# Kernel optimization log

Measured on AMD Instinct MI355X. Metric: run time of the kernel, lower is better.

## Reference

```python
import jax, jax.numpy as jnp
import numpy as np
import math

N, L, D = 1024, 32, 768
N_OUT, IN_DIM, OUT_DIM = 16, 64, 64
EPS = 1e-8


def setup_inputs() -> dict:
    key = jax.random.key(0)
    ks = jax.random.split(key, 4)
    x = jax.random.normal(ks[0], (N, L, D), jnp.float32)
    mask = jnp.ones((N, L), jnp.float32)
    scaled = lambda k, shape, fan: jax.random.normal(k, shape, jnp.float32) * (1.0 / np.sqrt(fan).astype(np.float32))
    Wscore = scaled(ks[1], (L, D, 1), D)
    Bscore = jnp.zeros((L, 1, 1), jnp.float32)
    Wcap = scaled(ks[2], (L, D, IN_DIM), D)
    Bcap = jnp.zeros((L, 1, IN_DIM), jnp.float32)
    Wvote = scaled(ks[3], (L, N_OUT, IN_DIM, OUT_DIM), IN_DIM)
    Bvote = jnp.zeros((L, N_OUT, 1, OUT_DIM), jnp.float32)
    beta_use = jnp.zeros((L, 1, 1, 1), jnp.float32)
    beta_ign = jnp.zeros((1, N_OUT, 1, 1), jnp.float32)
    return dict(x=x, mask=mask, Wscore=Wscore, Bscore=Bscore, Wcap=Wcap,
                Bcap=Bcap, Wvote=Wvote, Bvote=Bvote, beta_use=beta_use,
                beta_ign=beta_ign, iters=3)


def reference(x, mask, Wscore, Bscore, Wcap, Bcap, Wvote, Bvote, beta_use, beta_ign, iters):
    n_out = Wvote.shape[1]
    half_pi = np.float32(0.5 * math.pi)
    x_t = jnp.transpose(x, (1, 0, 2))                      # [L, N, D]
    a_in = jnp.matmul(x_t, Wscore) + Bscore                # [L, N, 1]
    mu_in = jax.nn.gelu(jnp.matmul(x_t, Wcap) + Bcap, approximate=False)  # [L, N, in_dim]
    f_a_in = jax.nn.sigmoid(a_in) * jnp.transpose(mask)[..., None]        # [L, N, 1]
    f_a_in = f_a_in[:, None, :, :]                         # [L, 1, N, 1]
    # votes: [L, n_out, N, out_dim] (einsum avoids materializing repeated mu_in)
    V = jnp.einsum('lni,lkio->lkno', mu_in, Wvote) + Bvote

    R = jnp.full((1, n_out, 1, 1), 1.0 / n_out, dtype=x.dtype)
    a_out = mu_out = var_out = None
    for t in range(iters):
        if t > 0:
            log_p = (-jnp.sum((V - mu_out[None]) ** 2 / (2.0 * var_out[None] + EPS), axis=-1)
                     - 1.0 - half_pi
                     - 0.5 * jnp.sum(jnp.log(var_out[None] + EPS), axis=-1))   # [L, n_out, N]
            R = jax.nn.softmax(jax.nn.log_sigmoid(a_out)[None] + log_p[..., None], axis=1)
        D_use = f_a_in * R                                  # [L, n_out, N, 1]
        D_ign = f_a_in - D_use
        a_out = jnp.sum(beta_use * D_use, axis=0) - jnp.sum(beta_ign * D_ign, axis=0)  # [n_out, N, 1]
        denom = jnp.sum(D_use, axis=0) + EPS                # [n_out, N, 1]
        mu_out = jnp.sum(D_use * V, axis=0) / denom         # [n_out, N, out_dim]
        var_out = jnp.sum(D_use * (V - mu_out[None]) ** 2, axis=0) / denom

    a_fin = jnp.transpose(a_out[..., 0])                    # [N, n_out]
    mu_fin = jnp.transpose(mu_out, (1, 0, 2))               # [N, n_out, out_dim]
    return a_fin, mu_fin
```

## Files before the change

### kernel.cpp

```cpp
#include <hip/hip_runtime.h>
#include <hip/hip_bf16.h>

#define L_DIM 32
#define N_DIM 1024
#define D_DIM 768
#define K_DIM 16
#define I_DIM 64
#define O_DIM 64
#define EPSF 1e-8f
#define PX 72

typedef unsigned short u16;
typedef __attribute__((ext_vector_type(8))) short short8;
typedef __attribute__((ext_vector_type(4))) float f32x4;
#define MFMA __builtin_amdgcn_mfma_f32_16x16x32_bf16

__device__ __forceinline__ float bf2f(u16 v) {
    union { unsigned int u; float f; } x; x.u = ((unsigned int)v) << 16; return x.f;
}
__device__ __forceinline__ u16 f2bf(float f) {
    union { float f; unsigned int u; } x; x.f = f;
    unsigned int u = x.u;
    u += 0x7FFFu + ((u >> 16) & 1u);
    return (u16)(u >> 16);
}
__device__ __forceinline__ void split2(float v, u16& h, u16& l) {
    u16 hh = f2bf(v);
    h = hh;
    l = f2bf(v - bf2f(hh));
}

__global__ __launch_bounds__(256) void prep_wcap(
    const float* __restrict__ W, u16* __restrict__ H, u16* __restrict__ Lo)
{
    const int l = blockIdx.y, d0 = blockIdx.x * 64, t = threadIdx.x;
    __shared__ float tile[64][65];
    #pragma unroll
    for (int p = 0; p < 4; p++) {
        int dd = p * 16 + (t >> 4), i4 = (t & 15) * 4;
        float4 v = *(const float4*)&W[((size_t)l * D_DIM + d0 + dd) * I_DIM + i4];
        tile[dd][i4] = v.x; tile[dd][i4+1] = v.y; tile[dd][i4+2] = v.z; tile[dd][i4+3] = v.w;
    }
    __syncthreads();
    #pragma unroll
    for (int p = 0; p < 4; p++) {
        int i = p * 16 + (t >> 4), dd0 = (t & 15) * 4;
        u16 h[4], lo[4];
        #pragma unroll
        for (int j = 0; j < 4; j++) split2(tile[dd0 + j][i], h[j], lo[j]);
        size_t base = ((size_t)l * I_DIM + i) * D_DIM + d0 + dd0;
        uint2 ph; ph.x = h[0] | ((unsigned)h[1] << 16); ph.y = h[2] | ((unsigned)h[3] << 16);
        uint2 pl; pl.x = lo[0] | ((unsigned)lo[1] << 16); pl.y = lo[2] | ((unsigned)lo[3] << 16);
        *(uint2*)&H[base] = ph;
        *(uint2*)&Lo[base] = pl;
    }
}

__global__ __launch_bounds__(256) void prep_wvote(
    const float* __restrict__ W, u16* __restrict__ H, u16* __restrict__ Lo)
{
    const int l = blockIdx.y, k = blockIdx.x, t = threadIdx.x;
    __shared__ float tile[64][65];
    #pragma unroll
    for (int p = 0; p < 4; p++) {
        int i = p * 16 + (t >> 4), o4 = (t & 15) * 4;
        float4 v = *(const float4*)&W[(((size_t)l * K_DIM + k) * I_DIM + i) * O_DIM + o4];
        tile[i][o4] = v.x; tile[i][o4+1] = v.y; tile[i][o4+2] = v.z; tile[i][o4+3] = v.w;
    }
    __syncthreads();
    #pragma unroll
    for (int p = 0; p < 4; p++) {
        int o = p * 16 + (t >> 4), i0 = (t & 15) * 4;
        u16 h[4], lo[4];
        #pragma unroll
        for (int j = 0; j < 4; j++) split2(tile[i0 + j][o], h[j], lo[j]);
        size_t base = (((size_t)l * K_DIM + k) * O_DIM + o) * I_DIM + i0;
        uint2 ph; ph.x = h[0] | ((unsigned)h[1] << 16); ph.y = h[2] | ((unsigned)h[3] << 16);
        uint2 pl; pl.x = lo[0] | ((unsigned)lo[1] << 16); pl.y = lo[2] | ((unsigned)lo[3] << 16);
        *(uint2*)&H[base] = ph;
        *(uint2*)&Lo[base] = pl;
    }
}

__global__ __launch_bounds__(256) void kernelA(
    const float* __restrict__ x, const float* __restrict__ mask,
    const float* __restrict__ Wscore, const float* __restrict__ Bscore,
    const u16* __restrict__ WcH, const u16* __restrict__ WcL,
    const float* __restrict__ Bcap,
    float* __restrict__ mu_out, float* __restrict__ fa_out,
    int nbase, int nchunk)
{
    const int l   = blockIdx.y;
    const int n0l = blockIdx.x * 32;
    const int t    = threadIdx.x;
    const int w    = t >> 6;
    const int lane = t & 63;
    const int quad = lane >> 4;
    const int ln16 = lane & 15;

    __shared__ u16 xh[32][PX], xl[32][PX];
    __shared__ float wsc_s[64];
    __shared__ float bcap_s[64];

    if (t < 64) bcap_s[t] = Bcap[l * I_DIM + t];

    f32x4 acc[2] = {{0.f,0.f,0.f,0.f},{0.f,0.f,0.f,0.f}};
    float apart = 0.f;

    for (int ch = 0; ch < 12; ch++) {
        const int k0 = ch * 64;
        __syncthreads();
        #pragma unroll
        for (int p = 0; p < 2; p++) {
            int n = p * 16 + (t >> 4), d0 = (t & 15) * 4;
            float4 v = *(const float4*)&x[((size_t)(nbase + n0l + n) * L_DIM + l) * D_DIM + k0 + d0];
            u16 h[4], lo[4];
            split2(v.x, h[0], lo[0]); split2(v.y, h[1], lo[1]);
            split2(v.z, h[2], lo[2]); split2(v.w, h[3], lo[3]);
            uint2 ph; ph.x = h[0] | ((unsigned)h[1] << 16); ph.y = h[2] | ((unsigned)h[3] << 16);
            uint2 pl; pl.x = lo[0] | ((unsigned)lo[1] << 16); pl.y = lo[2] | ((unsigned)lo[3] << 16);
            *(uint2*)&xh[n][d0] = ph;
            *(uint2*)&xl[n][d0] = pl;
        }
        if (t < 64) wsc_s[t] = Wscore[l * D_DIM + k0 + t];
        __syncthreads();

        {
            const int n = t >> 3, s8 = (t & 7) * 8;
            float ss = 0.f;
            #pragma unroll
            for (int j = 0; j < 8; j++) {
                int dd = s8 + j;
                ss += (bf2f(xh[n][dd]) + bf2f(xl[n][dd])) * wsc_s[dd];
            }
            apart += ss;
        }

        #pragma unroll
        for (int ks = 0; ks < 2; ks++) {
            const int kk = ks * 32;
            size_t wbase = ((size_t)l * I_DIM + (w * 16 + ln16)) * D_DIM + k0 + kk + quad * 8;
            short8 ah = *(const short8*)&WcH[wbase];
            short8 al = *(const short8*)&WcL[wbase];
            #pragma unroll
            for (int c = 0; c < 2; c++) {
                const int n = c * 16 + ln16;
                short8 bh = *(const short8*)&xh[n][kk + quad * 8];
                short8 bl = *(const short8*)&xl[n][kk + quad * 8];
                acc[c] = MFMA(ah, bh, acc[c], 0, 0, 0);
                acc[c] = MFMA(ah, bl, acc[c], 0, 0, 0);
                acc[c] = MFMA(al, bh, acc[c], 0, 0, 0);
            }
        }
    }

    apart += __shfl_xor(apart, 1, 64);
    apart += __shfl_xor(apart, 2, 64);
    apart += __shfl_xor(apart, 4, 64);
    if ((t & 7) == 0) {
        int n = t >> 3;
        float a = apart + Bscore[l];
        float sig = 1.f / (1.f + expf(-a));
        float m = mask[(size_t)(nbase + n0l + n) * L_DIM + l];
        fa_out[(size_t)l * nchunk + n0l + n] = sig * m;
    }

    #pragma unroll
    for (int c = 0; c < 2; c++) {
        const int n = c * 16 + ln16;
        const int i0 = w * 16 + quad * 4;
        float4 o;
        float* op = (float*)&o;
        #pragma unroll
        for (int r = 0; r < 4; r++) {
            float v = acc[c][r] + bcap_s[i0 + r];
            op[r] = 0.5f * v * (1.f + erff(v * 0.70710678118f));
        }
        *(float4*)&mu_out[((size_t)l * nchunk + n0l + n) * I_DIM + i0] = o;
    }
}

__global__ __launch_bounds__(256) void kernelB(
    const float* __restrict__ mu_in,
    const u16* __restrict__ WvH, const u16* __restrict__ WvL,
    const float* __restrict__ Bvote,
    float* __restrict__ V, int nchunk)
{
    const int l   = blockIdx.z;
    const int k   = blockIdx.y;
    const int n0l = blockIdx.x * 64;
    const int t    = threadIdx.x;
    const int w    = t >> 6;
    const int lane = t & 63;
    const int quad = lane >> 4;
    const int ln16 = lane & 15;

    __shared__ u16 mh[64][PX], ml[64][PX];
    __shared__ float bvote_s[64];

    if (t < 64) bvote_s[t] = Bvote[((size_t)l * K_DIM + k) * O_DIM + t];

    #pragma unroll
    for (int p = 0; p < 4; p++) {
        int n = p * 16 + (t >> 4), i0 = (t & 15) * 4;
        float4 v = *(const float4*)&mu_in[((size_t)l * nchunk + n0l + n) * I_DIM + i0];
        u16 h[4], lo[4];
        split2(v.x, h[0], lo[0]); split2(v.y, h[1], lo[1]);
        split2(v.z, h[2], lo[2]); split2(v.w, h[3], lo[3]);
        uint2 ph; ph.x = h[0] | ((unsigned)h[1] << 16); ph.y = h[2] | ((unsigned)h[3] << 16);
        uint2 pl; pl.x = lo[0] | ((unsigned)lo[1] << 16); pl.y = lo[2] | ((unsigned)lo[3] << 16);
        *(uint2*)&mh[n][i0] = ph;
        *(uint2*)&ml[n][i0] = pl;
    }
    __syncthreads();

    f32x4 acc[4] = {{0.f,0.f,0.f,0.f},{0.f,0.f,0.f,0.f},{0.f,0.f,0.f,0.f},{0.f,0.f,0.f,0.f}};

    #pragma unroll
    for (int ks = 0; ks < 2; ks++) {
        const int kk = ks * 32;
        size_t wbase = (((size_t)l * K_DIM + k) * O_DIM + (w * 16 + ln16)) * I_DIM + kk + quad * 8;
        short8 ah = *(const short8*)&WvH[wbase];
        short8 al = *(const short8*)&WvL[wbase];
        #pragma unroll
        for (int c = 0; c < 4; c++) {
            const int n = c * 16 + ln16;
            short8 bh = *(const short8*)&mh[n][kk + quad * 8];
            short8 bl = *(const short8*)&ml[n][kk + quad * 8];
            acc[c] = MFMA(ah, bh, acc[c], 0, 0, 0);
            acc[c] = MFMA(ah, bl, acc[c], 0, 0, 0);
            acc[c] = MFMA(al, bh, acc[c], 0, 0, 0);
        }
    }

    #pragma unroll
    for (int c = 0; c < 4; c++) {
        const int n = c * 16 + ln16;
        const int o0 = w * 16 + quad * 4;
        float4 o;
        o.x = acc[c][0] + bvote_s[o0];
        o.y = acc[c][1] + bvote_s[o0 + 1];
        o.z = acc[c][2] + bvote_s[o0 + 2];
        o.w = acc[c][3] + bvote_s[o0 + 3];
        *(float4*)&V[(((size_t)(n0l + n) * L_DIM + l) * K_DIM + k) * O_DIM + o0] = o;
    }
}

__global__ __launch_bounds__(256) void kernelC(
    const float* __restrict__ V, const float* __restrict__ fa_in,
    const float* __restrict__ beta_use, const float* __restrict__ beta_ign,
    const int* __restrict__ iters_p,
    float* __restrict__ out, int nbase, int nchunk)
{
    const int nl = blockIdx.x;
    const int ng = nbase + nl;
    const int t  = threadIdx.x;
    const int k  = t >> 4;
    const int og = (t & 15) << 2;
    int iters = iters_p[0];
    if (iters < 0 || iters > 16) iters = 3;

    __shared__ float fa_s[32];
    __shared__ float bu_s[32];
    __shared__ float R_s[32][17];
    __shared__ float sc_s[32][17];

    if (t < 32) {
        fa_s[t] = fa_in[(size_t)t * nchunk + nl];
        bu_s[t] = beta_use[t];
    }
    for (int idx = t; idx < 512; idx += 256)
        R_s[idx >> 4][idx & 15] = 1.f / 16.f;
    const float bi_k = beta_ign[k];

    const float* Vb = V + (size_t)nl * (L_DIM * K_DIM * O_DIM);
    float Vr[32][4];
    #pragma unroll
    for (int l = 0; l < 32; l++) {
        float4 v = *(const float4*)&Vb[(l * K_DIM + k) * O_DIM + og];
        Vr[l][0] = v.x; Vr[l][1] = v.y; Vr[l][2] = v.z; Vr[l][3] = v.w;
    }
    __syncthreads();

    float mu_r[4] = {0.f, 0.f, 0.f, 0.f};
    float var_r[4] = {0.f, 0.f, 0.f, 0.f};
    float a_r = 0.f;

    for (int it = 0; it < iters; it++) {
        if (it > 0) {
            float inv2v[4], lvp = 0.f;
            #pragma unroll
            for (int j = 0; j < 4; j++) {
                inv2v[j] = 1.f / (2.f * var_r[j] + EPSF);
                lvp += logf(var_r[j] + EPSF);
            }
            lvp += __shfl_xor(lvp, 1, 64);
            lvp += __shfl_xor(lvp, 2, 64);
            lvp += __shfl_xor(lvp, 4, 64);
            lvp += __shfl_xor(lvp, 8, 64);
            float ls = fminf(a_r, 0.f) - log1pf(expf(-fabsf(a_r)));
            const float cst = ls - 1.f - 1.57079632679f - 0.5f * lvp;
            #pragma unroll
            for (int l = 0; l < 32; l++) {
                float s = 0.f;
                #pragma unroll
                for (int j = 0; j < 4; j++) {
                    float d = Vr[l][j] - mu_r[j];
                    s += d * d * inv2v[j];
                }
                s = -s;
                s += __shfl_xor(s, 1, 64);
                s += __shfl_xor(s, 2, 64);
                s += __shfl_xor(s, 4, 64);
                s += __shfl_xor(s, 8, 64);
                if ((t & 15) == 0) sc_s[l][k] = s + cst;
            }
            __syncthreads();
            {
                const int lr = t >> 3;
                const int c2 = (t & 7) * 2;
                float s0 = sc_s[lr][c2], s1 = sc_s[lr][c2 + 1];
                float m = fmaxf(s0, s1);
                m = fmaxf(m, __shfl_xor(m, 1, 64));
                m = fmaxf(m, __shfl_xor(m, 2, 64));
                m = fmaxf(m, __shfl_xor(m, 4, 64));
                float e0 = expf(s0 - m), e1 = expf(s1 - m);
                float sum = e0 + e1;
                sum += __shfl_xor(sum, 1, 64);
                sum += __shfl_xor(sum, 2, 64);
                sum += __shfl_xor(sum, 4, 64);
                float inv = 1.f / sum;
                R_s[lr][c2]     = e0 * inv;
                R_s[lr][c2 + 1] = e1 * inv;
            }
            __syncthreads();
        }
        float denom = EPSF, a_acc = 0.f;
        float mu_a[4] = {0.f, 0.f, 0.f, 0.f};
        float v2_a[4] = {0.f, 0.f, 0.f, 0.f};
        #pragma unroll
        for (int l = 0; l < 32; l++) {
            float Du = fa_s[l] * R_s[l][k];
            denom += Du;
            a_acc += bu_s[l] * Du - bi_k * (fa_s[l] - Du);
            #pragma unroll
            for (int j = 0; j < 4; j++) {
                float dv = Du * Vr[l][j];
                mu_a[j] += dv;
                v2_a[j] += dv * Vr[l][j];
            }
        }
        float invd = 1.f / denom;
        #pragma unroll
        for (int j = 0; j < 4; j++) {
            mu_r[j] = mu_a[j] * invd;
            var_r[j] = fmaxf(v2_a[j] * invd - mu_r[j] * mu_r[j], 0.f);
        }
        a_r = a_acc;
    }

    if ((t & 15) == 0) out[(size_t)ng * K_DIM + k] = a_r;
    float4 o4;
    o4.x = mu_r[0]; o4.y = mu_r[1]; o4.z = mu_r[2]; o4.w = mu_r[3];
    *(float4*)&out[(size_t)N_DIM * K_DIM + ((size_t)ng * K_DIM + k) * O_DIM + og] = o4;
}

extern "C" void kernel_launch(void* const* d_in, const int* in_sizes, int n_in,
                              void* d_out, int out_size, void* d_ws, size_t ws_size,
                              hipStream_t stream) {
    (void)out_size;
    static const int EXP[11] = {25165824, 32768, 24576, 32, 1572864, 64,
                                2097152, 65536, 32, 16, 1};
    int mapi[11];
    bool used[64] = {false};
    for (int s = 0; s < 11; s++) {
        mapi[s] = (s < n_in) ? s : 0;
        for (int j = 0; j < n_in && j < 64; j++) {
            if (!used[j] && in_sizes[j] == EXP[s]) { mapi[s] = j; used[j] = true; break; }
        }
    }
    const float* x        = (const float*)d_in[mapi[0]];
    const float* mask     = (const float*)d_in[mapi[1]];
    const float* Wscore   = (const float*)d_in[mapi[2]];
    const float* Bscore   = (const float*)d_in[mapi[3]];
    const float* Wcap     = (const float*)d_in[mapi[4]];
    const float* Bcap     = (const float*)d_in[mapi[5]];
    const float* Wvote    = (const float*)d_in[mapi[6]];
    const float* Bvote    = (const float*)d_in[mapi[7]];
    const float* beta_use = (const float*)d_in[mapi[8]];
    const float* beta_ign = (const float*)d_in[mapi[9]];
    const int*   iters    = (const int*)d_in[mapi[10]];
    float* out = (float*)d_out;

    const size_t WCAP = (size_t)L_DIM * I_DIM * D_DIM;
    const size_t WVOT = (size_t)L_DIM * K_DIM * O_DIM * I_DIM;
    const size_t WBYTES = 2 * WCAP * 2 + 2 * WVOT * 2;

    int C = 64;
    {
        const int cands[5] = {1024, 512, 256, 128, 64};
        for (int i = 0; i < 5; i++) {
            size_t need = WBYTES + (size_t)cands[i] * (128 + 8192 + 131072);
            if (need <= ws_size) { C = cands[i]; break; }
        }
    }

    char* ws = (char*)d_ws;
    u16* WcH = (u16*)ws;
    u16* WcL = (u16*)(ws + WCAP * 2);
    u16* WvH = (u16*)(ws + WCAP * 4);
    u16* WvL = (u16*)(ws + WCAP * 4 + WVOT * 2);
    char* dyn = ws + WBYTES;
    float* fa = (float*)dyn;
    float* mu = (float*)(dyn + (size_t)128 * C);
    float* V  = (float*)(dyn + (size_t)128 * C + (size_t)8192 * C);

    prep_wcap<<<dim3(12, 32), 256, 0, stream>>>(Wcap, WcH, WcL);
    prep_wvote<<<dim3(16, 32), 256, 0, stream>>>(Wvote, WvH, WvL);

    for (int nbase = 0; nbase < N_DIM; nbase += C) {
        kernelA<<<dim3(C / 32, 32), 256, 0, stream>>>(
            x, mask, Wscore, Bscore, WcH, WcL, Bcap, mu, fa, nbase, C);
        kernelB<<<dim3(C / 64, 16, 32), 256, 0, stream>>>(
            mu, WvH, WvL, Bvote, V, C);
        kernelC<<<dim3(C), 256, 0, stream>>>(
            V, fa, beta_use, beta_ign, iters, out, nbase, C);
    }
}
```

Baseline: 299.1 us.

## Double-buffer kernelA x tiles, widen to 64 rows, transpose V layout

kernelA now processes 64 rows per block instead of 32, preloads the whole Wscore row into shared memory, and double-buffers the x tile so the next chunk's global load and bf16 split overlap the current chunk's MFMA work. This removes one barrier per chunk and halves how often each Wcap fragment is re-read per row. The V buffer layout moves from [n][l][k][o] to [l][k][n][o], which changes how kernelB writes and kernelC reads. In exchange, kernelA uses more shared memory and registers, and kernelC's per-row reads become strided across l and k.

Result: slower. 306.4 us (+2.4%).

```diff
diff --git a/kernel.cpp b/kernel.cpp
--- a/kernel.cpp
+++ b/kernel.cpp
@@ -91,47 +91,67 @@
     int nbase, int nchunk)
 {
     const int l   = blockIdx.y;
-    const int n0l = blockIdx.x * 32;
+    const int n0l = blockIdx.x * 64;
     const int t    = threadIdx.x;
     const int w    = t >> 6;
     const int lane = t & 63;
     const int quad = lane >> 4;
     const int ln16 = lane & 15;
 
-    __shared__ u16 xh[32][PX], xl[32][PX];
-    __shared__ float wsc_s[64];
+    __shared__ u16 xh[2][64][PX], xl[2][64][PX];
+    __shared__ float wsc_s[D_DIM];
     __shared__ float bcap_s[64];
 
+    for (int i = t; i < D_DIM; i += 256) wsc_s[i] = Wscore[l * D_DIM + i];
     if (t < 64) bcap_s[t] = Bcap[l * I_DIM + t];
 
-    f32x4 acc[2] = {{0.f,0.f,0.f,0.f},{0.f,0.f,0.f,0.f}};
+    const int sn = t >> 4;
+    const int sd = (t & 15) * 4;
+
+    #pragma unroll
+    for (int p = 0; p < 4; p++) {
+        int n = p * 16 + sn;
+        float4 v = *(const float4*)&x[((size_t)(nbase + n0l + n) * L_DIM + l) * D_DIM + sd];
+        u16 h[4], lo[4];
+        split2(v.x, h[0], lo[0]); split2(v.y, h[1], lo[1]);
+        split2(v.z, h[2], lo[2]); split2(v.w, h[3], lo[3]);
+        uint2 ph; ph.x = h[0] | ((unsigned)h[1] << 16); ph.y = h[2] | ((unsigned)h[3] << 16);
+        uint2 pl; pl.x = lo[0] | ((unsigned)lo[1] << 16); pl.y = lo[2] | ((unsigned)lo[3] << 16);
+        *(uint2*)&xh[0][n][sd] = ph;
+        *(uint2*)&xl[0][n][sd] = pl;
+    }
+    __syncthreads();
+
+    f32x4 acc[4] = {{0.f,0.f,0.f,0.f},{0.f,0.f,0.f,0.f},{0.f,0.f,0.f,0.f},{0.f,0.f,0.f,0.f}};
     float apart = 0.f;
 
     for (int ch = 0; ch < 12; ch++) {
+        const int buf = ch & 1;
         const int k0 = ch * 64;
-        __syncthreads();
-        #pragma unroll
-        for (int p = 0; p < 2; p++) {
-            int n = p * 16 + (t >> 4), d0 = (t & 15) * 4;
-            float4 v = *(const float4*)&x[((size_t)(nbase + n0l + n) * L_DIM + l) * D_DIM + k0 + d0];
-            u16 h[4], lo[4];
-            split2(v.x, h[0], lo[0]); split2(v.y, h[1], lo[1]);
-            split2(v.z, h[2], lo[2]); split2(v.w, h[3], lo[3]);
-            uint2 ph; ph.x = h[0] | ((unsigned)h[1] << 16); ph.y = h[2] | ((unsigned)h[3] << 16);
-            uint2 pl; pl.x = lo[0] | ((unsigned)lo[1] << 16); pl.y = lo[2] | ((unsigned)lo[3] << 16);
-            *(uint2*)&xh[n][d0] = ph;
-            *(uint2*)&xl[n][d0] = pl;
-        }
-        if (t < 64) wsc_s[t] = Wscore[l * D_DIM + k0 + t];
-        __syncthreads();
+
+        if (ch + 1 < 12) {
+            const int k1 = k0 + 64;
+            #pragma unroll
+            for (int p = 0; p < 4; p++) {
+                int n = p * 16 + sn;
+                float4 v = *(const float4*)&x[((size_t)(nbase + n0l + n) * L_DIM + l) * D_DIM + k1 + sd];
+                u16 h[4], lo[4];
+                split2(v.x, h[0], lo[0]); split2(v.y, h[1], lo[1]);
+                split2(v.z, h[2], lo[2]); split2(v.w, h[3], lo[3]);
+                uint2 ph; ph.x = h[0] | ((unsigned)h[1] << 16); ph.y = h[2] | ((unsigned)h[3] << 16);
+                uint2 pl; pl.x = lo[0] | ((unsigned)lo[1] << 16); pl.y = lo[2] | ((unsigned)lo[3] << 16);
+                *(uint2*)&xh[buf ^ 1][n][sd] = ph;
+                *(uint2*)&xl[buf ^ 1][n][sd] = pl;
+            }
+        }
 
         {
-            const int n = t >> 3, s8 = (t & 7) * 8;
+            const int fn = t >> 2, fs = (t & 3) * 16;
             float ss = 0.f;
             #pragma unroll
-            for (int j = 0; j < 8; j++) {
-                int dd = s8 + j;
-                ss += (bf2f(xh[n][dd]) + bf2f(xl[n][dd])) * wsc_s[dd];
+            for (int j = 0; j < 16; j++) {
+                int dd = fs + j;
+                ss += (bf2f(xh[buf][fn][dd]) + bf2f(xl[buf][fn][dd])) * wsc_s[k0 + dd];
             }
             apart += ss;
         }
@@ -143,22 +163,22 @@
             short8 ah = *(const short8*)&WcH[wbase];
             short8 al = *(const short8*)&WcL[wbase];
             #pragma unroll
-            for (int c = 0; c < 2; c++) {
+            for (int c = 0; c < 4; c++) {
                 const int n = c * 16 + ln16;
-                short8 bh = *(const short8*)&xh[n][kk + quad * 8];
-                short8 bl = *(const short8*)&xl[n][kk + quad * 8];
+                short8 bh = *(const short8*)&xh[buf][n][kk + quad * 8];
+                short8 bl = *(const short8*)&xl[buf][n][kk + quad * 8];
                 acc[c] = MFMA(ah, bh, acc[c], 0, 0, 0);
                 acc[c] = MFMA(ah, bl, acc[c], 0, 0, 0);
                 acc[c] = MFMA(al, bh, acc[c], 0, 0, 0);
             }
         }
+        __syncthreads();
     }
 
     apart += __shfl_xor(apart, 1, 64);
     apart += __shfl_xor(apart, 2, 64);
-    apart += __shfl_xor(apart, 4, 64);
-    if ((t & 7) == 0) {
-        int n = t >> 3;
+    if ((t & 3) == 0) {
+        int n = t >> 2;
         float a = apart + Bscore[l];
         float sig = 1.f / (1.f + expf(-a));
         float m = mask[(size_t)(nbase + n0l + n) * L_DIM + l];
@@ -166,7 +186,7 @@
     }
 
     #pragma unroll
-    for (int c = 0; c < 2; c++) {
+    for (int c = 0; c < 4; c++) {
         const int n = c * 16 + ln16;
         const int i0 = w * 16 + quad * 4;
         float4 o;
@@ -242,7 +262,7 @@
         o.y = acc[c][1] + bvote_s[o0 + 1];
         o.z = acc[c][2] + bvote_s[o0 + 2];
         o.w = acc[c][3] + bvote_s[o0 + 3];
-        *(float4*)&V[(((size_t)(n0l + n) * L_DIM + l) * K_DIM + k) * O_DIM + o0] = o;
+        *(float4*)&V[(((size_t)l * K_DIM + k) * nchunk + n0l + n) * O_DIM + o0] = o;
     }
 }
 
@@ -273,11 +293,10 @@
         R_s[idx >> 4][idx & 15] = 1.f / 16.f;
     const float bi_k = beta_ign[k];
 
-    const float* Vb = V + (size_t)nl * (L_DIM * K_DIM * O_DIM);
     float Vr[32][4];
     #pragma unroll
     for (int l = 0; l < 32; l++) {
-        float4 v = *(const float4*)&Vb[(l * K_DIM + k) * O_DIM + og];
+        float4 v = *(const float4*)&V[(((size_t)l * K_DIM + k) * nchunk + nl) * O_DIM + og];
         Vr[l][0] = v.x; Vr[l][1] = v.y; Vr[l][2] = v.z; Vr[l][3] = v.w;
     }
     __syncthreads();
@@ -419,7 +438,7 @@
     prep_wvote<<<dim3(16, 32), 256, 0, stream>>>(Wvote, WvH, WvL);
 
     for (int nbase = 0; nbase < N_DIM; nbase += C) {
-        kernelA<<<dim3(C / 32, 32), 256, 0, stream>>>(
+        kernelA<<<dim3(C / 64, 32), 256, 0, stream>>>(
             x, mask, Wscore, Bscore, WcH, WcL, Bcap, mu, fa, nbase, C);
         kernelB<<<dim3(C / 64, 16, 32), 256, 0, stream>>>(
             mu, WvH, WvL, Bvote, V, C);
```

## Double-buffer x tiles in kernelA, compute score in fp32, change V layout

Applied to the files above, without the earlier changes.

kernelA now prefetches the next 64-column slice of x into registers while MFMAs run on a double-buffered LDS tile, which removes one barrier per chunk. It also loads all of Wscore into LDS once and computes the score dot product from the fp32 registers instead of re-reading the bf16 hi/lo split. The hi/lo bf16 split now uses truncation in a packed helper instead of round-to-nearest, which slightly changes numerics. V is stored as [l][k][n][o] instead of [n][l][k][o], so kernelB writes contiguous rows while kernelC's per-block reads become strided across l.

New measurement: 296.5 us. About the same (-0.9%).

```diff
diff --git a/kernel.cpp b/kernel.cpp
--- a/kernel.cpp
+++ b/kernel.cpp
@@ -28,6 +28,21 @@
     u16 hh = f2bf(v);
     h = hh;
     l = f2bf(v - bf2f(hh));
+}
+__device__ __forceinline__ void store_split4(u16* ph, u16* pl, float4 v) {
+    unsigned u0 = __float_as_uint(v.x), u1 = __float_as_uint(v.y);
+    unsigned u2 = __float_as_uint(v.z), u3 = __float_as_uint(v.w);
+    uint2 H, L;
+    H.x = (u0 >> 16) | (u1 & 0xFFFF0000u);
+    H.y = (u2 >> 16) | (u3 & 0xFFFF0000u);
+    float l0 = v.x - __uint_as_float(u0 & 0xFFFF0000u);
+    float l1 = v.y - __uint_as_float(u1 & 0xFFFF0000u);
+    float l2 = v.z - __uint_as_float(u2 & 0xFFFF0000u);
+    float l3 = v.w - __uint_as_float(u3 & 0xFFFF0000u);
+    L.x = (__float_as_uint(l0) >> 16) | (__float_as_uint(l1) & 0xFFFF0000u);
+    L.y = (__float_as_uint(l2) >> 16) | (__float_as_uint(l3) & 0xFFFF0000u);
+    *(uint2*)ph = H;
+    *(uint2*)pl = L;
 }
 
 __global__ __launch_bounds__(256) void prep_wcap(
@@ -98,42 +113,44 @@
     const int quad = lane >> 4;
     const int ln16 = lane & 15;
 
-    __shared__ u16 xh[32][PX], xl[32][PX];
-    __shared__ float wsc_s[64];
+    __shared__ u16 xh[2][32][PX], xl[2][32][PX];
+    __shared__ float wsc_s[D_DIM];
     __shared__ float bcap_s[64];
 
+    for (int i = t; i < D_DIM; i += 256) wsc_s[i] = Wscore[l * D_DIM + i];
     if (t < 64) bcap_s[t] = Bcap[l * I_DIM + t];
 
+    const int sg = t >> 4;
+    const int sd = (t & 15) * 4;
+
+    const size_t xoff0 = ((size_t)(nbase + n0l + sg) * L_DIM + l) * D_DIM;
+    const size_t xoff1 = ((size_t)(nbase + n0l + 16 + sg) * L_DIM + l) * D_DIM;
+
+    float4 r0 = *(const float4*)&x[xoff0 + sd];
+    float4 r1 = *(const float4*)&x[xoff1 + sd];
+
+    __syncthreads();
+
     f32x4 acc[2] = {{0.f,0.f,0.f,0.f},{0.f,0.f,0.f,0.f}};
-    float apart = 0.f;
+    float fa0 = 0.f, fa1 = 0.f;
 
     for (int ch = 0; ch < 12; ch++) {
+        const int buf = ch & 1;
         const int k0 = ch * 64;
+
+        {
+            const float* wp = &wsc_s[k0 + sd];
+            fa0 += r0.x * wp[0] + r0.y * wp[1] + r0.z * wp[2] + r0.w * wp[3];
+            fa1 += r1.x * wp[0] + r1.y * wp[1] + r1.z * wp[2] + r1.w * wp[3];
+        }
+        store_split4(&xh[buf][sg][sd],      &xl[buf][sg][sd],      r0);
+        store_split4(&xh[buf][16 + sg][sd], &xl[buf][16 + sg][sd], r1);
         __syncthreads();
-        #pragma unroll
-        for (int p = 0; p < 2; p++) {
-            int n = p * 16 + (t >> 4), d0 = (t & 15) * 4;
-            float4 v = *(const float4*)&x[((size_t)(nbase + n0l + n) * L_DIM + l) * D_DIM + k0 + d0];
-            u16 h[4], lo[4];
-            split2(v.x, h[0], lo[0]); split2(v.y, h[1], lo[1]);
-            split2(v.z, h[2], lo[2]); split2(v.w, h[3], lo[3]);
-            uint2 ph; ph.x = h[0] | ((unsigned)h[1] << 16); ph.y = h[2] | ((unsigned)h[3] << 16);
-            uint2 pl; pl.x = lo[0] | ((unsigned)lo[1] << 16); pl.y = lo[2] | ((unsigned)lo[3] << 16);
-            *(uint2*)&xh[n][d0] = ph;
-            *(uint2*)&xl[n][d0] = pl;
-        }
-        if (t < 64) wsc_s[t] = Wscore[l * D_DIM + k0 + t];
-        __syncthreads();
-
-        {
-            const int n = t >> 3, s8 = (t & 7) * 8;
-            float ss = 0.f;
-            #pragma unroll
-            for (int j = 0; j < 8; j++) {
-                int dd = s8 + j;
-                ss += (bf2f(xh[n][dd]) + bf2f(xl[n][dd])) * wsc_s[dd];
-            }
-            apart += ss;
+
+        if (ch + 1 < 12) {
+            const int k1 = k0 + 64;
+            r0 = *(const float4*)&x[xoff0 + k1 + sd];
+            r1 = *(const float4*)&x[xoff1 + k1 + sd];
         }
 
         #pragma unroll
@@ -145,8 +162,8 @@
             #pragma unroll
             for (int c = 0; c < 2; c++) {
                 const int n = c * 16 + ln16;
-                short8 bh = *(const short8*)&xh[n][kk + quad * 8];
-                short8 bl = *(const short8*)&xl[n][kk + quad * 8];
+                short8 bh = *(const short8*)&xh[buf][n][kk + quad * 8];
+                short8 bl = *(const short8*)&xl[buf][n][kk + quad * 8];
                 acc[c] = MFMA(ah, bh, acc[c], 0, 0, 0);
                 acc[c] = MFMA(ah, bl, acc[c], 0, 0, 0);
                 acc[c] = MFMA(al, bh, acc[c], 0, 0, 0);
@@ -154,15 +171,24 @@
         }
     }
 
-    apart += __shfl_xor(apart, 1, 64);
-    apart += __shfl_xor(apart, 2, 64);
-    apart += __shfl_xor(apart, 4, 64);
-    if ((t & 7) == 0) {
-        int n = t >> 3;
-        float a = apart + Bscore[l];
-        float sig = 1.f / (1.f + expf(-a));
-        float m = mask[(size_t)(nbase + n0l + n) * L_DIM + l];
-        fa_out[(size_t)l * nchunk + n0l + n] = sig * m;
+    fa0 += __shfl_xor(fa0, 1, 64); fa1 += __shfl_xor(fa1, 1, 64);
+    fa0 += __shfl_xor(fa0, 2, 64); fa1 += __shfl_xor(fa1, 2, 64);
+    fa0 += __shfl_xor(fa0, 4, 64); fa1 += __shfl_xor(fa1, 4, 64);
+    fa0 += __shfl_xor(fa0, 8, 64); fa1 += __shfl_xor(fa1, 8, 64);
+    if ((t & 15) == 0) {
+        float bs = Bscore[l];
+        {
+            float a = fa0 + bs;
+            float sig = 1.f / (1.f + expf(-a));
+            float m = mask[(size_t)(nbase + n0l + sg) * L_DIM + l];
+            fa_out[(size_t)l * nchunk + n0l + sg] = sig * m;
+        }
+        {
+            float a = fa1 + bs;
+            float sig = 1.f / (1.f + expf(-a));
+            float m = mask[(size_t)(nbase + n0l + 16 + sg) * L_DIM + l];
+            fa_out[(size_t)l * nchunk + n0l + 16 + sg] = sig * m;
+        }
     }
 
     #pragma unroll
@@ -204,13 +230,7 @@
     for (int p = 0; p < 4; p++) {
         int n = p * 16 + (t >> 4), i0 = (t & 15) * 4;
         float4 v = *(const float4*)&mu_in[((size_t)l * nchunk + n0l + n) * I_DIM + i0];
-        u16 h[4], lo[4];
-        split2(v.x, h[0], lo[0]); split2(v.y, h[1], lo[1]);
-        split2(v.z, h[2], lo[2]); split2(v.w, h[3], lo[3]);
-        uint2 ph; ph.x = h[0] | ((unsigned)h[1] << 16); ph.y = h[2] | ((unsigned)h[3] << 16);
-        uint2 pl; pl.x = lo[0] | ((unsigned)lo[1] << 16); pl.y = lo[2] | ((unsigned)lo[3] << 16);
-        *(uint2*)&mh[n][i0] = ph;
-        *(uint2*)&ml[n][i0] = pl;
+        store_split4(&mh[n][i0], &ml[n][i0], v);
     }
     __syncthreads();
 
@@ -242,7 +262,7 @@
         o.y = acc[c][1] + bvote_s[o0 + 1];
         o.z = acc[c][2] + bvote_s[o0 + 2];
         o.w = acc[c][3] + bvote_s[o0 + 3];
-        *(float4*)&V[(((size_t)(n0l + n) * L_DIM + l) * K_DIM + k) * O_DIM + o0] = o;
+        *(float4*)&V[(((size_t)l * K_DIM + k) * nchunk + n0l + n) * O_DIM + o0] = o;
     }
 }
 
@@ -273,11 +293,10 @@
         R_s[idx >> 4][idx & 15] = 1.f / 16.f;
     const float bi_k = beta_ign[k];
 
-    const float* Vb = V + (size_t)nl * (L_DIM * K_DIM * O_DIM);
     float Vr[32][4];
     #pragma unroll
     for (int l = 0; l < 32; l++) {
-        float4 v = *(const float4*)&Vb[(l * K_DIM + k) * O_DIM + og];
+        float4 v = *(const float4*)&V[(((size_t)l * K_DIM + k) * nchunk + nl) * O_DIM + og];
         Vr[l][0] = v.x; Vr[l][1] = v.y; Vr[l][2] = v.z; Vr[l][3] = v.w;
     }
     __syncthreads();
```
